# Kernel optimization log

Measured on AMD Instinct MI355X. Metric: run time of the kernel, lower is better.

Reference implementation:

```python
import jax, jax.numpy as jnp
import numpy as np
from jax import lax

# Static config (idx == 0: horizontal stripes -> overlap along width)
B, H, W = 32, 56, 56
C, NH = 128, 4
HD = C // NH          # 32
S = 7                 # split_size
POS = 2
KY, KX = S, S * (2 * POS + 1)   # 7, 35 (k/v window)
SCALE = HD ** -0.5
NPH = H // S          # 8 window rows
WP = W + 2 * POS * S  # padded width = 84
NPW = (WP - KX) // S + 1  # 8 window cols
NW = NPH * NPW        # 64 windows per image


def setup_inputs() -> dict:
    key = jax.random.key(0)
    k1, k2, k3 = jax.random.split(key, 3)
    qkv = jax.random.normal(k1, (3, B, H * W, C), dtype=jnp.float32)
    w_lepe = jax.random.normal(k2, (3, 3, 1, C), dtype=jnp.float32) * 0.1
    b_lepe = jax.random.normal(k3, (C,), dtype=jnp.float32) * 0.1
    return {"qkv": qkv, "w_lepe": w_lepe, "b_lepe": b_lepe}


def _forward(qkv, w_lepe, b_lepe):
    q, k, v = qkv.reshape(3, B, H, W, C)

    # ---- q: non-overlapping SxS windows, head-major channel split ----
    qw = q.reshape(B, NPH, S, NPW, S, C).transpose(0, 1, 3, 2, 4, 5)
    qw = qw.reshape(B, NW, S * S, C)
    qh = qw.reshape(B, NW, S * S, NH, HD).transpose(0, 1, 3, 2, 4)  # [B,NW,NH,49,HD]

    # ---- k/v: pad width by POS*S each side, overlapping KYxKX windows ----
    def window_kv(t):
        tp = jnp.pad(t, ((0, 0), (0, 0), (POS * S, POS * S), (0, 0)))  # [B,H,WP,C]
        # rows are non-overlapping (stride == KY); cols overlap (stride S, width KX)
        t5 = tp.reshape(B, NPH, KY, WP, C)
        col = jnp.arange(NPW)[:, None] * S + jnp.arange(KX)[None, :]   # [NPW,KX]
        tw = t5[:, :, :, col, :]                 # [B,NPH,KY,NPW,KX,C]
        tw = tw.transpose(0, 1, 3, 2, 4, 5)      # [B,NPH,NPW,KY,KX,C]
        return tw.reshape(B, NW, KY * KX, C)

    kw = window_kv(k)
    vw = window_kv(v)
    kh = kw.reshape(B, NW, KY * KX, NH, HD).transpose(0, 1, 3, 2, 4)  # [B,NW,NH,245,HD]
    vh = vw.reshape(B, NW, KY * KX, NH, HD).transpose(0, 1, 3, 2, 4)

    # ---- LePE: depthwise 3x3 conv on the center SxS slice of each v window ----
    v_img = vw.reshape(B * NW, KY, KX, C)
    center = v_img[:, :, POS * S:(POS + 1) * S, :]                    # [B*NW,S,S,C]
    lepe = lax.conv_general_dilated(
        center, w_lepe, window_strides=(1, 1), padding='SAME',
        dimension_numbers=('NHWC', 'HWIO', 'NHWC'), feature_group_count=C)
    lepe = lepe + b_lepe
    lepeh = lepe.reshape(B, NW, S * S, NH, HD).transpose(0, 1, 3, 2, 4)  # [B,NW,NH,49,HD]

    # ---- tiny per-window attention: softmax(q k^T) v + lepe ----
    sim = jnp.einsum('bwhqd,bwhkd->bwhqk', qh * SCALE, kh)  # [B,NW,NH,49,245]
    attn = jax.nn.softmax(sim, axis=-1)
    out = jnp.einsum('bwhqk,bwhkd->bwhqd', attn, vh) + lepeh

    # ---- merge heads (head-major) and un-window ----
    out = out.transpose(0, 1, 3, 2, 4).reshape(B, NW, S * S, C)
    out = out.reshape(B, NPH, NPW, S, S, C).transpose(0, 1, 3, 2, 4, 5)
    return out.reshape(B, H * W, C)


def reference(qkv, w_lepe, b_lepe):
    return _forward(qkv, w_lepe, b_lepe)
```

## Files before the change

kernel.cpp:

```cpp
#include <hip/hip_runtime.h>
#include <hip/hip_bf16.h>

#define B_ 32
#define H_ 56
#define W_ 56
#define C_ 128
#define NH_ 4
#define HD_ 32
#define S_ 7
#define KXW 35
#define NKEY 245
#define SCL2E 0.25503486f

typedef short short8 __attribute__((ext_vector_type(8)));
typedef float f32x4 __attribute__((ext_vector_type(4)));
typedef unsigned u32x2 __attribute__((ext_vector_type(2)));

#define KSTR 40
#define VSTR 264
#define PSTR 136
#define PBLK 2176
#define SK_OFF 0
#define SV_OFF 10240
#define SM_TOT 18960

__device__ __forceinline__ unsigned pk2(float a, float b) {
  __hip_bfloat162 t = __float22bfloat162_rn(float2{a, b});
  unsigned r;
  __builtin_memcpy(&r, &t, 4);
  return r;
}
__device__ __forceinline__ float bf2f(unsigned short u) {
  unsigned x = ((unsigned)u) << 16;
  return __builtin_bit_cast(float, x);
}

__global__ __launch_bounds__(256, 4) void lepe_attn(
    const float* __restrict__ qkv, const float* __restrict__ w_lepe,
    const float* __restrict__ b_lepe, float* __restrict__ out) {
  __shared__ __align__(16) unsigned short sm[SM_TOT];

  const int n = blockIdx.x;
  const int h  = n & 3;
  const int wx = (n >> 2) & 7;
  const int wy = (n >> 5) & 7;
  const int b  = n >> 8;
  const int tid  = threadIdx.x;
  const int lane = tid & 63;
  const int wave = tid >> 6;
  const int c0 = h * HD_;

  const float* Qg = qkv;
  const float* Kg = qkv + (size_t)B_ * H_ * W_ * C_;
  const float* Vg = Kg + (size_t)B_ * H_ * W_ * C_;
  const size_t bimg = (size_t)b * H_ * W_ * C_;

  const int quad = lane >> 4;
  const int cc = lane & 15;
  const int mt = wave;

  const int mrow = mt * 16 + cc;
  float4 qa = {0.f, 0.f, 0.f, 0.f}, qb = {0.f, 0.f, 0.f, 0.f};
  if (mrow < 49) {
    const int y = mrow / 7, x = mrow - (mrow / 7) * 7;
    const float* qp = Qg + bimg + ((size_t)((wy * 7 + y) * W_ + wx * 7 + x)) * C_ + c0 + quad * 8;
    qa = *reinterpret_cast<const float4*>(qp);
    qb = *reinterpret_cast<const float4*>(qp + 4);
  }

  for (int i = tid; i < 256 * 8; i += 256) {
    const int j = i >> 3, dg = i & 7;
    float4 kv = {0.f, 0.f, 0.f, 0.f}, vv = {0.f, 0.f, 0.f, 0.f};
    if (j < NKEY) {
      const int ky = j / KXW, kx = j - (j / KXW) * KXW;
      const int xx = wx * 7 + kx - 14;
      if (xx >= 0 && xx < W_) {
        const size_t gi = bimg + ((size_t)((wy * 7 + ky) * W_ + xx)) * C_ + c0 + dg * 4;
        kv = *reinterpret_cast<const float4*>(Kg + gi);
        vv = *reinterpret_cast<const float4*>(Vg + gi);
      }
    }
    const unsigned k01 = pk2(kv.x, kv.y), k23 = pk2(kv.z, kv.w);
    *reinterpret_cast<uint2*>(sm + SK_OFF + j * KSTR + dg * 4) = uint2{k01, k23};
    const unsigned v01 = pk2(vv.x, vv.y), v23 = pk2(vv.z, vv.w);
    const int d = dg * 4;
    unsigned short* vp = sm + SV_OFF + d * VSTR + dg * 40 + j;
    vp[0 * VSTR] = (unsigned short)v01;
    vp[1 * VSTR] = (unsigned short)(v01 >> 16);
    vp[2 * VSTR] = (unsigned short)v23;
    vp[3 * VSTR] = (unsigned short)(v23 >> 16);
  }

  union { unsigned u[4]; short8 s; } afru;
  afru.u[0] = pk2(qa.x * SCL2E, qa.y * SCL2E);
  afru.u[1] = pk2(qa.z * SCL2E, qa.w * SCL2E);
  afru.u[2] = pk2(qb.x * SCL2E, qb.y * SCL2E);
  afru.u[3] = pk2(qb.z * SCL2E, qb.w * SCL2E);
  const short8 afr = afru.s;

  __syncthreads();

  f32x4 acc[16];
#pragma unroll
  for (int nt = 0; nt < 16; ++nt) {
    short8 bfr = *reinterpret_cast<const short8*>(sm + SK_OFF + (nt * 16 + cc) * KSTR + quad * 8);
    f32x4 z = {0.f, 0.f, 0.f, 0.f};
    acc[nt] = __builtin_amdgcn_mfma_f32_16x16x32_bf16(bfr, afr, z, 0, 0, 0);
  }

  float sum = 0.f;
#pragma unroll
  for (int nt = 0; nt < 16; ++nt) {
#pragma unroll
    for (int r = 0; r < 4; ++r) {
      float e = __builtin_amdgcn_exp2f(acc[nt][r]);
      if (nt == 15 && (quad * 4 + r) >= 5) e = 0.f;
      acc[nt][r] = e;
      sum += e;
    }
  }
  sum += __shfl_xor(sum, 16, 64);
  sum += __shfl_xor(sum, 32, 64);
  const float rv = __builtin_amdgcn_rcpf(sum);

  __syncthreads();

  unsigned short* pw = sm + SK_OFF + mt * PBLK;
  f32x4 o0 = {0.f, 0.f, 0.f, 0.f}, o1 = {0.f, 0.f, 0.f, 0.f};
#pragma unroll
  for (int half = 0; half < 2; ++half) {
#pragma unroll
    for (int nt = 0; nt < 8; ++nt) {
      const f32x4 a = acc[half * 8 + nt];
      *reinterpret_cast<u32x2*>(pw + cc * PSTR + nt * 16 + quad * 4) =
          (u32x2){pk2(a[0] * rv, a[1] * rv), pk2(a[2] * rv, a[3] * rv)};
    }
#pragma unroll
    for (int ks = 0; ks < 4; ++ks) {
      short8 pfr = *reinterpret_cast<const short8*>(pw + cc * PSTR + ks * 32 + quad * 8);
      const int keyo = half * 128 + ks * 32 + quad * 8;
      short8 v0 = *reinterpret_cast<const short8*>(
          sm + SV_OFF + cc * VSTR + (cc >> 2) * 40 + keyo);
      short8 v1 = *reinterpret_cast<const short8*>(
          sm + SV_OFF + (16 + cc) * VSTR + (4 + (cc >> 2)) * 40 + keyo);
      o0 = __builtin_amdgcn_mfma_f32_16x16x32_bf16(pfr, v0, o0, 0, 0, 0);
      o1 = __builtin_amdgcn_mfma_f32_16x16x32_bf16(pfr, v1, o1, 0, 0, 0);
    }
  }

#pragma unroll
  for (int half = 0; half < 2; ++half) {
    const int d = cc + half * 16;
    const unsigned short* vrow = sm + SV_OFF + d * VSTR + ((d >> 2) & 7) * 40;
    float wl[9];
#pragma unroll
    for (int t = 0; t < 9; ++t) wl[t] = w_lepe[t * C_ + c0 + d];
    const float bl = b_lepe[c0 + d];
    const f32x4 o = half ? o1 : o0;
#pragma unroll
    for (int r = 0; r < 4; ++r) {
      const int p = mt * 16 + quad * 4 + r;
      if (p < 49) {
        const int y = p / 7, x = p - (p / 7) * 7;
        float l = bl;
#pragma unroll
        for (int dy = -1; dy <= 1; ++dy) {
          const int yy = y + dy;
          if (yy < 0 || yy >= 7) continue;
#pragma unroll
          for (int dx = -1; dx <= 1; ++dx) {
            const int xx = x + dx;
            if (xx < 0 || xx >= 7) continue;
            const int key = yy * KXW + 14 + xx;
            l += wl[(dy + 1) * 3 + (dx + 1)] * bf2f(vrow[key]);
          }
        }
        const float res = o[r] + l;
        out[bimg + ((size_t)((wy * 7 + y) * W_ + wx * 7 + x)) * C_ + c0 + d] = res;
      }
    }
  }
}

extern "C" void kernel_launch(void* const* d_in, const int* in_sizes, int n_in,
                              void* d_out, int out_size, void* d_ws, size_t ws_size,
                              hipStream_t stream) {
  const float* qkv    = (const float*)d_in[0];
  const float* w_lepe = (const float*)d_in[1];
  const float* b_lepe = (const float*)d_in[2];
  float* out = (float*)d_out;
  lepe_attn<<<8192, 256, 0, stream>>>(qkv, w_lepe, b_lepe, out);
}
```

Baseline: 304.4 us.

## Batch K/V global loads per thread and vectorize transposed V LDS stores

Each thread now loads four consecutive keys for two key blocks up front, increasing outstanding global loads. V is transposed into shared memory with packed 8-byte writes instead of four scalar 16-bit stores per element. Softmax normalization moves from the probability tile to the final output, using a lane shuffle to fetch each row's reciprocal sum. Loading everything up front raises register pressure, which may hurt occupancy.

```diff
diff --git a/kernel.cpp b/kernel.cpp
--- a/kernel.cpp
+++ b/kernel.cpp
@@ -14,6 +14,7 @@
 
 typedef short short8 __attribute__((ext_vector_type(8)));
 typedef float f32x4 __attribute__((ext_vector_type(4)));
+typedef float f4 __attribute__((ext_vector_type(4)));
 typedef unsigned u32x2 __attribute__((ext_vector_type(2)));
 
 #define KSTR 40
@@ -59,43 +60,80 @@
   const int cc = lane & 15;
   const int mt = wave;
 
+  const f4 z4 = {0.f, 0.f, 0.f, 0.f};
+
   const int mrow = mt * 16 + cc;
-  float4 qa = {0.f, 0.f, 0.f, 0.f}, qb = {0.f, 0.f, 0.f, 0.f};
+  f4 qa = z4, qb = z4;
   if (mrow < 49) {
     const int y = mrow / 7, x = mrow - (mrow / 7) * 7;
     const float* qp = Qg + bimg + ((size_t)((wy * 7 + y) * W_ + wx * 7 + x)) * C_ + c0 + quad * 8;
-    qa = *reinterpret_cast<const float4*>(qp);
-    qb = *reinterpret_cast<const float4*>(qp + 4);
-  }
-
-  for (int i = tid; i < 256 * 8; i += 256) {
-    const int j = i >> 3, dg = i & 7;
-    float4 kv = {0.f, 0.f, 0.f, 0.f}, vv = {0.f, 0.f, 0.f, 0.f};
-    if (j < NKEY) {
-      const int ky = j / KXW, kx = j - (j / KXW) * KXW;
-      const int xx = wx * 7 + kx - 14;
-      if (xx >= 0 && xx < W_) {
-        const size_t gi = bimg + ((size_t)((wy * 7 + ky) * W_ + xx)) * C_ + c0 + dg * 4;
-        kv = *reinterpret_cast<const float4*>(Kg + gi);
-        vv = *reinterpret_cast<const float4*>(Vg + gi);
-      }
-    }
-    const unsigned k01 = pk2(kv.x, kv.y), k23 = pk2(kv.z, kv.w);
-    *reinterpret_cast<uint2*>(sm + SK_OFF + j * KSTR + dg * 4) = uint2{k01, k23};
-    const unsigned v01 = pk2(vv.x, vv.y), v23 = pk2(vv.z, vv.w);
-    const int d = dg * 4;
-    unsigned short* vp = sm + SV_OFF + d * VSTR + dg * 40 + j;
-    vp[0 * VSTR] = (unsigned short)v01;
-    vp[1 * VSTR] = (unsigned short)(v01 >> 16);
-    vp[2 * VSTR] = (unsigned short)v23;
-    vp[3 * VSTR] = (unsigned short)(v23 >> 16);
+    qa = *reinterpret_cast<const f4*>(qp);
+    qb = *reinterpret_cast<const f4*>(qp + 4);
+  }
+
+  const int t8 = tid >> 3, dg = tid & 7;
+  const int jb0 = 4 * t8, jb1 = jb0 + 128;
+
+  f4 kvA[4], vvA[4], kvB[4], vvB[4];
+#pragma unroll
+  for (int kk = 0; kk < 4; ++kk) {
+    const int j = jb0 + kk;
+    const int ky = j / KXW, kx = j - (j / KXW) * KXW;
+    const int xx = wx * 7 + kx - 14;
+    kvA[kk] = z4; vvA[kk] = z4;
+    if (xx >= 0 && xx < W_) {
+      const size_t gi = bimg + ((size_t)((wy * 7 + ky) * W_ + xx)) * C_ + c0 + dg * 4;
+      kvA[kk] = *reinterpret_cast<const f4*>(Kg + gi);
+      vvA[kk] = *reinterpret_cast<const f4*>(Vg + gi);
+    }
+  }
+#pragma unroll
+  for (int kk = 0; kk < 4; ++kk) {
+    const int j = jb1 + kk;
+    const int ky = j / KXW, kx = j - (j / KXW) * KXW;
+    const int xx = wx * 7 + kx - 14;
+    kvB[kk] = z4; vvB[kk] = z4;
+    if (j < NKEY && xx >= 0 && xx < W_) {
+      const size_t gi = bimg + ((size_t)((wy * 7 + ky) * W_ + xx)) * C_ + c0 + dg * 4;
+      kvB[kk] = *reinterpret_cast<const f4*>(Kg + gi);
+      vvB[kk] = *reinterpret_cast<const f4*>(Vg + gi);
+    }
+  }
+
+#pragma unroll
+  for (int kk = 0; kk < 4; ++kk) {
+    *reinterpret_cast<uint2*>(sm + SK_OFF + (jb0 + kk) * KSTR + dg * 4) =
+        uint2{pk2(kvA[kk][0], kvA[kk][1]), pk2(kvA[kk][2], kvA[kk][3])};
+  }
+  {
+    unsigned short* vb = sm + SV_OFF + dg * 40 + jb0;
+#pragma unroll
+    for (int dd = 0; dd < 4; ++dd) {
+      const unsigned lo = pk2(vvA[0][dd], vvA[1][dd]);
+      const unsigned hi = pk2(vvA[2][dd], vvA[3][dd]);
+      *reinterpret_cast<u32x2*>(vb + (dg * 4 + dd) * VSTR) = (u32x2){lo, hi};
+    }
+  }
+#pragma unroll
+  for (int kk = 0; kk < 4; ++kk) {
+    *reinterpret_cast<uint2*>(sm + SK_OFF + (jb1 + kk) * KSTR + dg * 4) =
+        uint2{pk2(kvB[kk][0], kvB[kk][1]), pk2(kvB[kk][2], kvB[kk][3])};
+  }
+  {
+    unsigned short* vb = sm + SV_OFF + dg * 40 + jb1;
+#pragma unroll
+    for (int dd = 0; dd < 4; ++dd) {
+      const unsigned lo = pk2(vvB[0][dd], vvB[1][dd]);
+      const unsigned hi = pk2(vvB[2][dd], vvB[3][dd]);
+      *reinterpret_cast<u32x2*>(vb + (dg * 4 + dd) * VSTR) = (u32x2){lo, hi};
+    }
   }
 
   union { unsigned u[4]; short8 s; } afru;
-  afru.u[0] = pk2(qa.x * SCL2E, qa.y * SCL2E);
-  afru.u[1] = pk2(qa.z * SCL2E, qa.w * SCL2E);
-  afru.u[2] = pk2(qb.x * SCL2E, qb.y * SCL2E);
-  afru.u[3] = pk2(qb.z * SCL2E, qb.w * SCL2E);
+  afru.u[0] = pk2(qa[0] * SCL2E, qa[1] * SCL2E);
+  afru.u[1] = pk2(qa[2] * SCL2E, qa[3] * SCL2E);
+  afru.u[2] = pk2(qb[0] * SCL2E, qb[1] * SCL2E);
+  afru.u[3] = pk2(qb[2] * SCL2E, qb[3] * SCL2E);
   const short8 afr = afru.s;
 
   __syncthreads();
@@ -133,7 +171,7 @@
     for (int nt = 0; nt < 8; ++nt) {
       const f32x4 a = acc[half * 8 + nt];
       *reinterpret_cast<u32x2*>(pw + cc * PSTR + nt * 16 + quad * 4) =
-          (u32x2){pk2(a[0] * rv, a[1] * rv), pk2(a[2] * rv, a[3] * rv)};
+          (u32x2){pk2(a[0], a[1]), pk2(a[2], a[3])};
     }
 #pragma unroll
     for (int ks = 0; ks < 4; ++ks) {
@@ -148,6 +186,10 @@
     }
   }
 
+  float rv4[4];
+#pragma unroll
+  for (int r = 0; r < 4; ++r) rv4[r] = __shfl(rv, quad * 4 + r, 64);
+
 #pragma unroll
   for (int half = 0; half < 2; ++half) {
     const int d = cc + half * 16;
@@ -175,8 +217,8 @@
             l += wl[(dy + 1) * 3 + (dx + 1)] * bf2f(vrow[key]);
           }
         }
-        const float res = o[r] + l;
-        out[bimg + ((size_t)((wy * 7 + y) * W_ + wx * 7 + x)) * C_ + c0 + d] = res;
+        out[bimg + ((size_t)((wy * 7 + y) * W_ + wx * 7 + x)) * C_ + c0 + d] =
+            o[r] * rv4[r] + l;
       }
     }
   }
```

Result: faster. 282.2 us (-7.3%).
